# Optimization experiments

Hardware: AMD Instinct MI355X
Metric: run time of the kernel (lower is better)

Reference implementation:

```python
import math
import jax, jax.numpy as jnp
from jax import lax
import numpy as np

B, CIN, COUT, K, SD, NCLS, H, W = 8, 512, 512, 3, 512, 35, 64, 64
EPS_DEMOD = 1e-8
EPS_IN = 1e-5  # torch InstanceNorm2d default eps


def _equal_linear(x, w, b):
    # EqualLinear: F.linear(x, w * (1/sqrt(in_dim))) + b  (lr_mul=1)
    return x @ (w.T * (1.0 / math.sqrt(w.shape[1]))) + b


def setup_inputs() -> dict:
    key = jax.random.key(0)
    ks = jax.random.split(key, 8)
    return {
        "input": jax.random.normal(ks[0], (B, CIN, H, W), jnp.float32),
        "style": jax.random.normal(ks[1], (B, SD), jnp.float32),
        "class_style": jax.random.normal(ks[2], (NCLS, SD), jnp.float32),
        "weight": jax.random.normal(ks[3], (1, COUT, CIN, K, K), jnp.float32),
        "mod_w": jax.random.normal(ks[4], (CIN, SD), jnp.float32),
        "mod_b": jnp.ones((CIN,), jnp.float32),  # bias_init=1
        "cw_w": jax.random.normal(ks[5], (COUT, SD), jnp.float32),
        "cw_b": jnp.ones((COUT,), jnp.float32),
        "cb_w": jax.random.normal(ks[6], (COUT, SD), jnp.float32),
        "cb_b": jnp.ones((COUT,), jnp.float32),
        "label_class_dict": jax.random.randint(ks[7], (B, H, W), 0, NCLS),
    }


def reference(input, style, class_style, weight, mod_w, mod_b, cw_w, cw_b, cb_w, cb_b, label_class_dict):
    scale = 1.0 / math.sqrt(CIN * K * K)
    pad = K // 2

    # per-sample style modulation of weights
    s = _equal_linear(style, mod_w, mod_b)                 # [B, CIN]
    w = scale * weight * s[:, None, :, None, None]         # [B, COUT, CIN, K, K]
    demod = lax.rsqrt(jnp.sum(w * w, axis=(2, 3, 4)) + EPS_DEMOD)  # [B, COUT]
    w = w * demod[:, :, None, None, None]

    # grouped conv (groups = batch) == vmap of per-sample conv
    def conv_one(x, wb):  # x [CIN,H,W], wb [COUT,CIN,K,K]
        return lax.conv_general_dilated(
            x[None], wb, window_strides=(1, 1), padding=[(pad, pad), (pad, pad)],
            dimension_numbers=("NCHW", "OIHW", "NCHW"))[0]

    out = jax.vmap(conv_one)(input, w)                     # [B, COUT, H, W]

    # param-free instance norm (biased variance, no affine)
    mu = out.mean(axis=(2, 3), keepdims=True)
    var = out.var(axis=(2, 3), keepdims=True)
    out = (out - mu) * lax.rsqrt(var + EPS_IN)

    # CLADE per-class affine from class_style, gathered via label map
    cw = _equal_linear(class_style, cw_w, cw_b)            # [NCLS, COUT]
    cb = _equal_linear(class_style, cb_w, cb_b)            # [NCLS, COUT]
    class_weight = jnp.transpose(cw[label_class_dict], (0, 3, 1, 2))  # [B,COUT,H,W]
    class_bias = jnp.transpose(cb[label_class_dict], (0, 3, 1, 2))
    return out * class_weight + class_bias
```

## Files before the change

### kernel.cpp

```cpp
#include <hip/hip_runtime.h>

typedef unsigned short u16;
typedef unsigned int u32;
typedef __attribute__((ext_vector_type(8))) short short8;
typedef __attribute__((ext_vector_type(4))) float floatx4;

typedef const u32 __attribute__((address_space(1))) glb_u32;
typedef u32 __attribute__((address_space(3))) lds_u32;

__device__ inline float bf2f(u16 h) {
  union { u32 u; float f; } v; v.u = ((u32)h) << 16; return v.f;
}
__device__ inline u16 f2bf(float f) {
  union { float f; u32 u; } v; v.f = f;
  u32 u = v.u;
  return (u16)((u + 0x7fffu + ((u >> 16) & 1u)) >> 16);
}
__device__ inline float ldf(const void* p, int i, int isbf) {
  return isbf ? bf2f(((const u16*)p)[i]) : ((const float*)p)[i];
}
__device__ inline void gl16(const void* g, void* l) {
  __builtin_amdgcn_global_load_lds((glb_u32*)g, (lds_u32*)l, 16, 0, 0);
}

__global__ __launch_bounds__(256) void prep_kernel(
    const void* __restrict__ style, const void* __restrict__ class_style,
    const void* __restrict__ weight,
    const void* __restrict__ mod_w, const void* __restrict__ mod_b,
    const void* __restrict__ cw_w, const void* __restrict__ cw_b,
    const void* __restrict__ cb_w, const void* __restrict__ cb_b,
    const void* __restrict__ x,
    float* __restrict__ s, float* __restrict__ cw, float* __restrict__ cb,
    u16* __restrict__ wT, float* __restrict__ wsqT2, u16* __restrict__ xT) {
  __shared__ float smem[4608];
  __shared__ int cnt;
  const int t = threadIdx.x;

  if (t == 0) cnt = 0;
  __syncthreads();
  {
    u32 v = ((const u32*)weight)[1024 + t];
    int e = (v >> 7) & 0xFF;
    if (e >= 96 && e <= 160) atomicAdd(&cnt, 1);
  }
  __syncthreads();
  const int isbf = (cnt >= 154) ? 1 : 0;
  const int bid = blockIdx.x;

  if (bid < 78) {
    int row = bid;
    const void *vec, *wm, *bias; float* out; int voff;
    if (row < 8)        { vec = style;       voff = row*512;      wm = mod_w; bias = mod_b; out = s  + row*512; }
    else if (row < 43)  { vec = class_style; voff = (row-8)*512;  wm = cw_w;  bias = cw_b;  out = cw + (row-8)*512; }
    else                { vec = class_style; voff = (row-43)*512; wm = cb_w;  bias = cb_b;  out = cb + (row-43)*512; }
    float* v = smem;
    for (int i = t; i < 512; i += 256) v[i] = ldf(vec, voff + i, isbf);
    __syncthreads();
    const float inv = 0.04419417382415922f;
    for (int o = t; o < 512; o += 256) {
      float acc = 0.f;
      if (isbf) {
        for (int k = 0; k < 512; ++k) acc += bf2f(((const u16*)wm)[o*512 + k]) * v[k];
      } else {
        const float4* wr = (const float4*)((const float*)wm + o*512);
        for (int k = 0; k < 128; ++k) {
          float4 p = wr[k];
          acc += p.x*v[k*4+0] + p.y*v[k*4+1] + p.z*v[k*4+2] + p.w*v[k*4+3];
        }
      }
      out[o] = acc * inv + ldf(bias, o, isbf);
    }
  } else if (bid < 590) {
    const int co = bid - 78;
    const int ctb = co >> 6, col = co & 63;
    float* wsmem = smem;
    for (int i = t; i < 4608; i += 256)
      wsmem[i] = ldf(weight, co*4608 + i, isbf);
    __syncthreads();
    for (int ci = t; ci < 512; ci += 256) {
      float sq = 0.f;
      const int ck = ci >> 5, q = (ci >> 3) & 3, e = ci & 7;
      #pragma unroll
      for (int tap = 0; tap < 9; ++tap) {
        float fv = wsmem[ci*9 + tap];
        sq += fv*fv;
        wT[((size_t)(ck*8 + ctb)*2304 + (tap*4 + q)*64 + col)*8 + e] = f2bf(fv);
      }
      wsqT2[(size_t)co*512 + ci] = sq;
    }
  } else {
    const int r = bid - 590;
    const int ck = r & 15, h = (r >> 4) & 63, b = r >> 10;
    float* sv = smem;
    float* sl = smem + 512;
    for (int i = t; i < 512; i += 256) sv[i] = ldf(style, b*512 + i, isbf);
    __syncthreads();
    const int lane = t & 63, wv = t >> 6;
    const float inv = 0.04419417382415922f;
    #pragma unroll
    for (int p = 0; p < 8; ++p) {
      const int row = p*4 + wv;
      const int ci = ck*32 + row;
      float partial = 0.f;
      if (isbf) {
        const u16* wr = (const u16*)mod_w + (size_t)ci*512 + lane*8;
        #pragma unroll
        for (int k = 0; k < 8; ++k) partial += bf2f(wr[k]) * sv[lane*8 + k];
      } else {
        const float4* wr = (const float4*)((const float*)mod_w + (size_t)ci*512 + lane*8);
        float4 p0 = wr[0], p1 = wr[1];
        partial += p0.x*sv[lane*8+0] + p0.y*sv[lane*8+1] + p0.z*sv[lane*8+2] + p0.w*sv[lane*8+3]
                 + p1.x*sv[lane*8+4] + p1.y*sv[lane*8+5] + p1.z*sv[lane*8+6] + p1.w*sv[lane*8+7];
      }
      #pragma unroll
      for (int off = 1; off < 64; off <<= 1) partial += __shfl_xor(partial, off, 64);
      if (lane == 0) sl[row] = partial * inv + ldf(mod_b, ci, isbf);
    }
    __syncthreads();
    const int w = t & 63, cq = t >> 6;
    float f[8];
    #pragma unroll
    for (int j = 0; j < 8; ++j) {
      float xv = ldf(x, (((b*512) + ck*32 + cq*8 + j)*64 + h)*64 + w, isbf);
      f[j] = xv * sl[cq*8 + j];
    }
    u32 outp[4];
    #pragma unroll
    for (int i = 0; i < 4; ++i)
      outp[i] = (u32)f2bf(f[2*i]) | ((u32)f2bf(f[2*i+1]) << 16);
    uint4 po = {outp[0], outp[1], outp[2], outp[3]};
    *(uint4*)&xT[((size_t)(((b*16 + ck)*64 + h)*256) + t)*8] = po;
  }
}

__global__ __launch_bounds__(512, 2) void conv_kernel(const u16* __restrict__ xT, const u16* __restrict__ wT,
                                                      float* __restrict__ y, float* __restrict__ part) {
  __shared__ __align__(16) u16 xs[18*4*67*8];
  __shared__ __align__(16) u16 wsm[2*2304*8];
  const int tid = threadIdx.x;
  const int lane = tid & 63;
  const int wid = tid >> 6;
  const int bid = blockIdx.x;
  const int b = bid & 7, ctb = (bid >> 3) & 7, hb = bid >> 6;
  const int ct0 = ctb * 64;
  const int h0 = hb * 16;
  const int m = lane & 15, qd = lane >> 4;

  {
    uint4 z = {0,0,0,0};
    for (int i = tid; i < 4824; i += 512) *(uint4*)&xs[i*8] = z;
  }

  floatx4 acc[4][8];
  #pragma unroll
  for (int i = 0; i < 4; ++i) {
    #pragma unroll
    for (int j = 0; j < 8; ++j) acc[i][j] = (floatx4)(0.f);
  }

  #define STAGE_X(ckn)                                                                     \
    for (int sl = wid; sl < 72; sl += 8) {                                                 \
      int dr = sl >> 2, q = sl & 3;                                                        \
      int hin = h0 + dr - 1;                                                               \
      if (hin >= 0 && hin <= 63) {                                                         \
        const u16* src = xT + ((size_t)(((b*16 + (ckn))*64 + hin)*256 + q*64 + lane))*8;   \
        gl16(src, &xs[((dr*4 + q)*67 + 1)*8]);                                             \
      }                                                                                    \
    }
  #define STAGE_W(ckn, bn)                                                                 \
    for (int j = wid; j < 36; j += 8) {                                                    \
      const u16* src = wT + ((size_t)(((ckn)*8 + ctb)*2304 + j*64 + lane))*8;              \
      gl16(src, &wsm[((bn)*2304 + j*64)*8]);                                               \
    }

  __syncthreads();
  STAGE_W(0, 0);

  for (int ck = 0; ck < 16; ++ck) {
    const int buf = ck & 1;
    __syncthreads();

    STAGE_X(ck);
    asm volatile("s_waitcnt vmcnt(0)" ::: "memory");
    __syncthreads();

    if (ck < 15) STAGE_W(ck + 1, buf ^ 1);

    const u16* wb = &wsm[buf*2304*8];
    #pragma unroll
    for (int tap = 0; tap < 9; ++tap) {
      const int k1 = tap / 3, k2 = tap - k1*3;
      short8 af[4], bfr[8];
      #pragma unroll
      for (int mi = 0; mi < 4; ++mi)
        af[mi] = *(const short8*)&wb[((tap*4 + qd)*64 + mi*16 + m)*8];
      #pragma unroll
      for (int hh = 0; hh < 2; ++hh) {
        const int dr = wid*2 + hh + k1;
        #pragma unroll
        for (int nw = 0; nw < 4; ++nw)
          bfr[hh*4 + nw] = *(const short8*)&xs[((dr*4 + qd)*67 + nw*16 + m + k2)*8];
      }
      #pragma unroll
      for (int ni = 0; ni < 8; ++ni) {
        #pragma unroll
        for (int mi = 0; mi < 4; ++mi)
          acc[mi][ni] = __builtin_amdgcn_mfma_f32_16x16x32_bf16(af[mi], bfr[ni], acc[mi][ni], 0, 0, 0);
      }
    }
  }
  #undef STAGE_X
  #undef STAGE_W

  #pragma unroll
  for (int mi = 0; mi < 4; ++mi) {
    #pragma unroll
    for (int hh = 0; hh < 2; ++hh) {
      const int h = h0 + wid*2 + hh;
      #pragma unroll
      for (int nw = 0; nw < 4; ++nw) {
        #pragma unroll
        for (int r = 0; r < 4; ++r) {
          int co = ct0 + mi*16 + qd*4 + r;
          int w = nw*16 + m;
          y[(size_t)(((b*512) + co)*64 + h)*64 + w] = acc[mi][hh*4 + nw][r];
        }
      }
    }
  }

  float s1[16], s2[16];
  #pragma unroll
  for (int mi = 0; mi < 4; ++mi) {
    #pragma unroll
    for (int r = 0; r < 4; ++r) {
      float a = 0.f, aa = 0.f;
      #pragma unroll
      for (int ni = 0; ni < 8; ++ni) {
        float v = acc[mi][ni][r];
        a += v; aa += v*v;
      }
      s1[mi*4+r] = a; s2[mi*4+r] = aa;
    }
  }
  #pragma unroll
  for (int off = 1; off < 16; off <<= 1) {
    #pragma unroll
    for (int i = 0; i < 16; ++i) {
      s1[i] += __shfl_xor(s1[i], off, 64);
      s2[i] += __shfl_xor(s2[i], off, 64);
    }
  }
  __syncthreads();
  float* red = (float*)xs;
  if (m == 0) {
    #pragma unroll
    for (int mi = 0; mi < 4; ++mi) {
      #pragma unroll
      for (int r = 0; r < 4; ++r) {
        int co = mi*16 + qd*4 + r;
        red[(wid*64 + co)*2 + 0] = s1[mi*4+r];
        red[(wid*64 + co)*2 + 1] = s2[mi*4+r];
      }
    }
  }
  __syncthreads();
  if (tid < 128) {
    int co = tid >> 1, which = tid & 1;
    float v = 0.f;
    #pragma unroll
    for (int w8 = 0; w8 < 8; ++w8) v += red[(w8*64 + co)*2 + which];
    part[(size_t)(((b*4 + hb)*512) + ct0 + co)*2 + which] = v;
  }
}

__global__ __launch_bounds__(256) void epi_kernel(float* __restrict__ y, const float* __restrict__ part,
                                                  const float* __restrict__ s, const float* __restrict__ wsqT2,
                                                  const float* __restrict__ cw, const float* __restrict__ cb,
                                                  const int* __restrict__ label) {
  const int bc = blockIdx.x;
  const int b = bc >> 9, co = bc & 511;
  const int t = threadIdx.x;
  __shared__ float tabw[35], tabb[35];
  __shared__ float redp[4];
  __shared__ float2 msh;
  if (t < 35) { tabw[t] = cw[t*512 + co]; tabb[t] = cb[t*512 + co]; }

  const float* sb = s + b*512;
  const float* wq = wsqT2 + (size_t)co*512;
  float ep;
  {
    float s0 = sb[t], s1v = sb[t + 256];
    ep = s0*s0*wq[t] + s1v*s1v*wq[t + 256];
  }
  #pragma unroll
  for (int off = 1; off < 64; off <<= 1) ep += __shfl_xor(ep, off, 64);
  if ((t & 63) == 0) redp[t >> 6] = ep;
  __syncthreads();
  if (t == 0) {
    float SS = redp[0] + redp[1] + redp[2] + redp[3];
    float S = 0.f, Q = 0.f;
    const float2* pv = (const float2*)part;
    #pragma unroll
    for (int hb = 0; hb < 4; ++hb) {
      float2 p = pv[(size_t)((b*4 + hb)*512) + co];
      S += p.x; Q += p.y;
    }
    float mval = S * (1.f/4096.f);
    float var = fmaxf(Q * (1.f/4096.f) - mval*mval, 0.f);
    float eps = 1e-5f*SS + 4.608e-10f;
    msh = make_float2(mval, rsqrtf(var + eps));
  }
  __syncthreads();
  const float mval = msh.x, is = msh.y;

  float* yp = y + (size_t)bc*4096 + t*16;
  const int* lp = label + b*4096 + t*16;
  #pragma unroll
  for (int u = 0; u < 4; ++u) {
    float4 v = *(const float4*)(yp + u*4);
    int4 l = *(const int4*)(lp + u*4);
    float4 o;
    o.x = (v.x - mval)*is*tabw[l.x] + tabb[l.x];
    o.y = (v.y - mval)*is*tabw[l.y] + tabb[l.y];
    o.z = (v.z - mval)*is*tabw[l.z] + tabb[l.z];
    o.w = (v.w - mval)*is*tabw[l.w] + tabb[l.w];
    *(float4*)(yp + u*4) = o;
  }
}

extern "C" void kernel_launch(void* const* d_in, const int* in_sizes, int n_in,
                              void* d_out, int out_size, void* d_ws, size_t ws_size,
                              hipStream_t stream) {
  (void)in_sizes; (void)n_in; (void)out_size; (void)ws_size;
  const void* input       = d_in[0];
  const void* style       = d_in[1];
  const void* class_style = d_in[2];
  const void* weight      = d_in[3];
  const void* mod_w       = d_in[4];
  const void* mod_b       = d_in[5];
  const void* cw_w        = d_in[6];
  const void* cw_b        = d_in[7];
  const void* cb_w        = d_in[8];
  const void* cb_b        = d_in[9];
  const int* label        = (const int*)d_in[10];
  float* y = (float*)d_out;

  char* ws = (char*)d_ws;
  u16*   xT    = (u16*)  (ws + 0);
  u16*   wT    = (u16*)  (ws + 33554432);
  float* wsqT2 = (float*)(ws + 38273024);
  float* s     = (float*)(ws + 39321600);
  float* cw    = (float*)(ws + 39337984);
  float* cb    = (float*)(ws + 39409664);
  float* part  = (float*)(ws + 39481344);

  hipLaunchKernelGGL(prep_kernel, dim3(8782), dim3(256), 0, stream,
                     style, class_style, weight, mod_w, mod_b, cw_w, cw_b, cb_w, cb_b,
                     input, s, cw, cb, wT, wsqT2, xT);
  hipLaunchKernelGGL(conv_kernel, dim3(256), dim3(512), 0, stream, xT, wT, y, part);
  hipLaunchKernelGGL(epi_kernel, dim3(4096), dim3(256), 0, stream, y, part, s, wsqT2, cw, cb, label);
}
```

Baseline: 326.0 us.

## Prefetch next input chunk into registers during MFMA loop; restructure style-mod reduction

The conv kernel now loads the next channel chunk of the transposed input into registers before the current chunk's MFMA loop. It writes that data to LDS after the compute, so global latency overlaps with math instead of stalling at the top of each iteration. The prep kernel's style-modulation dot product is also reorganised: each thread reduces a 64-element segment, then partials are combined via LDS instead of wave shuffles. The prefetch costs 9 uint4 registers per thread, which raises register pressure on top of the 128 accumulator floats and may reduce occupancy or cause spills.

Result: slower. 443.6 us (+36.1%).

```diff
diff --git a/kernel.cpp b/kernel.cpp
--- a/kernel.cpp
+++ b/kernel.cpp
@@ -92,29 +92,36 @@
     const int r = bid - 590;
     const int ck = r & 15, h = (r >> 4) & 63, b = r >> 10;
     float* sv = smem;
-    float* sl = smem + 512;
+    float* pr = smem + 512;
+    float* sl = smem + 768;
     for (int i = t; i < 512; i += 256) sv[i] = ldf(style, b*512 + i, isbf);
     __syncthreads();
-    const int lane = t & 63, wv = t >> 6;
     const float inv = 0.04419417382415922f;
-    #pragma unroll
-    for (int p = 0; p < 8; ++p) {
-      const int row = p*4 + wv;
+    {
+      const int row = t >> 3, seg = t & 7;
       const int ci = ck*32 + row;
+      const float* svp = sv + seg*64;
       float partial = 0.f;
       if (isbf) {
-        const u16* wr = (const u16*)mod_w + (size_t)ci*512 + lane*8;
-        #pragma unroll
-        for (int k = 0; k < 8; ++k) partial += bf2f(wr[k]) * sv[lane*8 + k];
+        const u16* wr = (const u16*)mod_w + (size_t)ci*512 + seg*64;
+        #pragma unroll
+        for (int k = 0; k < 64; ++k) partial += bf2f(wr[k]) * svp[k];
       } else {
-        const float4* wr = (const float4*)((const float*)mod_w + (size_t)ci*512 + lane*8);
-        float4 p0 = wr[0], p1 = wr[1];
-        partial += p0.x*sv[lane*8+0] + p0.y*sv[lane*8+1] + p0.z*sv[lane*8+2] + p0.w*sv[lane*8+3]
-                 + p1.x*sv[lane*8+4] + p1.y*sv[lane*8+5] + p1.z*sv[lane*8+6] + p1.w*sv[lane*8+7];
-      }
-      #pragma unroll
-      for (int off = 1; off < 64; off <<= 1) partial += __shfl_xor(partial, off, 64);
-      if (lane == 0) sl[row] = partial * inv + ldf(mod_b, ci, isbf);
+        const float4* wr = (const float4*)((const float*)mod_w + (size_t)ci*512 + seg*64);
+        #pragma unroll
+        for (int k = 0; k < 16; ++k) {
+          float4 p = wr[k];
+          partial += p.x*svp[k*4+0] + p.y*svp[k*4+1] + p.z*svp[k*4+2] + p.w*svp[k*4+3];
+        }
+      }
+      pr[t] = partial;
+    }
+    __syncthreads();
+    if (t < 32) {
+      float a = 0.f;
+      #pragma unroll
+      for (int g = 0; g < 8; ++g) a += pr[t*8 + g];
+      sl[t] = a * inv + ldf(mod_b, ck*32 + t, isbf);
     }
     __syncthreads();
     const int w = t & 63, cq = t >> 6;
@@ -158,34 +165,42 @@
     for (int j = 0; j < 8; ++j) acc[i][j] = (floatx4)(0.f);
   }
 
-  #define STAGE_X(ckn)                                                                     \
-    for (int sl = wid; sl < 72; sl += 8) {                                                 \
-      int dr = sl >> 2, q = sl & 3;                                                        \
-      int hin = h0 + dr - 1;                                                               \
-      if (hin >= 0 && hin <= 63) {                                                         \
-        const u16* src = xT + ((size_t)(((b*16 + (ckn))*64 + hin)*256 + q*64 + lane))*8;   \
-        gl16(src, &xs[((dr*4 + q)*67 + 1)*8]);                                             \
-      }                                                                                    \
-    }
+  uint4 xreg[9];
+
   #define STAGE_W(ckn, bn)                                                                 \
     for (int j = wid; j < 36; j += 8) {                                                    \
       const u16* src = wT + ((size_t)(((ckn)*8 + ctb)*2304 + j*64 + lane))*8;              \
       gl16(src, &wsm[((bn)*2304 + j*64)*8]);                                               \
     }
+  #define XLOAD(ckn)                                                                       \
+    _Pragma("unroll") for (int j = 0; j < 9; ++j) {                                        \
+      int sl = wid + j*8; int dr = sl >> 2, q = sl & 3;                                    \
+      int hin = h0 + dr - 1;                                                               \
+      if (hin >= 0 && hin <= 63)                                                           \
+        xreg[j] = *(const uint4*)(xT + ((size_t)(((b*16 + (ckn))*64 + hin)*256 + q*64 + lane))*8); \
+    }
+  #define XWRITE()                                                                         \
+    _Pragma("unroll") for (int j = 0; j < 9; ++j) {                                        \
+      int sl = wid + j*8; int dr = sl >> 2, q = sl & 3;                                    \
+      int hin = h0 + dr - 1;                                                               \
+      if (hin >= 0 && hin <= 63)                                                           \
+        *(uint4*)&xs[(((dr*4 + q)*67) + 1 + lane)*8] = xreg[j];                            \
+    }
 
   __syncthreads();
   STAGE_W(0, 0);
+  XLOAD(0);
+  XWRITE();
+  asm volatile("s_waitcnt vmcnt(0)" ::: "memory");
+  __syncthreads();
 
   for (int ck = 0; ck < 16; ++ck) {
     const int buf = ck & 1;
-    __syncthreads();
-
-    STAGE_X(ck);
-    asm volatile("s_waitcnt vmcnt(0)" ::: "memory");
-    __syncthreads();
-
-    if (ck < 15) STAGE_W(ck + 1, buf ^ 1);
-
+    if (ck < 15) {
+      STAGE_W(ck + 1, buf ^ 1);
+      XLOAD(ck + 1);
+    }
+    __builtin_amdgcn_sched_barrier(0);
     const u16* wb = &wsm[buf*2304*8];
     #pragma unroll
     for (int tap = 0; tap < 9; ++tap) {
@@ -208,9 +223,16 @@
           acc[mi][ni] = __builtin_amdgcn_mfma_f32_16x16x32_bf16(af[mi], bfr[ni], acc[mi][ni], 0, 0, 0);
       }
     }
-  }
-  #undef STAGE_X
+    __syncthreads();
+    if (ck < 15) {
+      XWRITE();
+      asm volatile("s_waitcnt vmcnt(0)" ::: "memory");
+      __syncthreads();
+    }
+  }
   #undef STAGE_W
+  #undef XLOAD
+  #undef XWRITE
 
   #pragma unroll
   for (int mi = 0; mi < 4; ++mi) {
@@ -251,7 +273,6 @@
       s2[i] += __shfl_xor(s2[i], off, 64);
     }
   }
-  __syncthreads();
   float* red = (float*)xs;
   if (m == 0) {
     #pragma unroll
```
